# Optimization experiments

Measured on AMD Instinct MI355X. Metric: run time of the kernel, lower is better.

The kernel has to match this reference:

```python
import jax, jax.numpy as jnp
import numpy as np

TEMPERATURE = 0.1
WEIGHT = 0.1
EPS = 1e-12  # F.normalize clamp_min eps

B = 512   # number of reactions (batches)
G = 128   # atoms per reaction per side (uniform groups)
D = 256   # feature dim


def setup_inputs() -> dict:
    key = jax.random.key(0)
    k1, k2, k3, k4 = jax.random.split(key, 4)
    preds = jax.random.normal(k1, (B,), dtype=jnp.float32)
    y = jax.random.normal(k2, (B,), dtype=jnp.float32)
    reactant_features = jax.random.normal(k3, (B * G, D), dtype=jnp.float32)
    product_features = jax.random.normal(k4, (B * G, D), dtype=jnp.float32)
    # sorted, uniform-size groups: [0]*G, [1]*G, ...
    batch_idx = jnp.repeat(jnp.arange(B, dtype=jnp.int64), G)
    return {
        "preds": preds,
        "y": y,
        "reactant_features": reactant_features,
        "product_features": product_features,
        "reactant_batch_indices": batch_idx,
        "product_batch_indices": batch_idx,
    }


def _l2_normalize(x):
    # matches F.normalize(p=2, dim=1): x / max(||x||, eps)
    n = jnp.sqrt(jnp.sum(x * x, axis=-1, keepdims=True))
    return x / jnp.maximum(n, EPS)


def reference(preds, y, reactant_features, product_features,
              reactant_batch_indices, product_batch_indices):
    # MSE with reduction='sum'
    mse_loss = jnp.sum((preds - y) ** 2)

    # groups are uniform and sorted -> per-batch gather == reshape
    nb = int(reactant_batch_indices[-1]) + 1          # number of unique batches
    g = reactant_features.shape[0] // nb
    d = reactant_features.shape[1]
    r = reactant_features.reshape(nb, g, d)
    p = product_features.reshape(nb, g, d)

    rn = _l2_normalize(r)
    pn = _l2_normalize(p)
    # per-batch similarity [nb, g, g]
    sim = jnp.einsum('bgd,bhd->bgh', rn, pn) / TEMPERATURE

    # cross_entropy with labels = arange(g), mean over rows (torch default)
    lse = jax.scipy.special.logsumexp(sim, axis=-1)   # [nb, g]
    diag = jnp.einsum('bgg->bg', sim)                 # logits at true labels
    ce_per_batch = jnp.mean(lse - diag, axis=-1)      # [nb]
    contrastive_loss = jnp.mean(ce_per_batch)         # sum over batches / nb

    return mse_loss + WEIGHT * contrastive_loss
```

## Files before the change

### kernel.cpp

```cpp
#include <hip/hip_runtime.h>
#include <math.h>

#define BATCH 512
#define G 128
#define D 256
#define QROWS 32
#define LRP 264

typedef __attribute__((ext_vector_type(8))) short short8;
typedef __attribute__((ext_vector_type(4))) float f32x4;
typedef __attribute__((ext_vector_type(4))) int  i32x4;

__device__ __forceinline__ unsigned int pack2bf16(float a, float b) {
    unsigned int ua = __float_as_uint(a);
    unsigned int ub = __float_as_uint(b);
    ua = (ua + 0x7FFFu + ((ua >> 16) & 1u)) >> 16;
    ub = (ub + 0x7FFFu + ((ub >> 16) & 1u)) >> 16;
    return ua | (ub << 16);
}

__global__ __launch_bounds__(512, 4)
void fused_kernel(const float* __restrict__ rfeat,
                  const float* __restrict__ pfeat,
                  const float* __restrict__ preds,
                  const float* __restrict__ yv,
                  float* __restrict__ out)
{
    const int b = blockIdx.x;
    const float* rb = rfeat + (size_t)b * (G * D);
    const float* pb = pfeat + (size_t)b * (G * D);

    __shared__ unsigned short qs[2][QROWS * LRP];
    __shared__ float inv_r[G];
    __shared__ float inv_p[G];
    __shared__ float red[8];

    const int tid  = threadIdx.x;
    const int lane = tid & 63;
    const int wv   = tid >> 6;
    const int lg   = lane >> 4;
    const int lc   = lane & 15;

    const int srow = tid >> 4;
    const int sc4  = tid & 15;

    float4 pq0[4], pq1[4];
#pragma unroll
    for (int j = 0; j < 4; ++j)
        pq0[j] = *reinterpret_cast<const float4*>(pb + (0 * QROWS + srow) * D + (sc4 + 16 * j) * 4);
#pragma unroll
    for (int j = 0; j < 4; ++j)
        pq1[j] = *reinterpret_cast<const float4*>(pb + (1 * QROWS + srow) * D + (sc4 + 16 * j) * 4);

    short8 afr[8];
    float nrsum = 0.f;
    const float* rptr = rb + (wv * 16 + lc) * D + lg * 8;
#pragma unroll
    for (int ks = 0; ks < 8; ++ks) {
        float4 x0 = *reinterpret_cast<const float4*>(rptr + ks * 32);
        float4 x1 = *reinterpret_cast<const float4*>(rptr + ks * 32 + 4);
        nrsum += x0.x*x0.x + x0.y*x0.y + x0.z*x0.z + x0.w*x0.w
               + x1.x*x1.x + x1.y*x1.y + x1.z*x1.z + x1.w*x1.w;
        i32x4 pk = { (int)pack2bf16(x0.x, x0.y), (int)pack2bf16(x0.z, x0.w),
                     (int)pack2bf16(x1.x, x1.y), (int)pack2bf16(x1.z, x1.w) };
        union { i32x4 i; short8 s; } u; u.i = pk;
        afr[ks] = u.s;
    }
    nrsum += __shfl_xor(nrsum, 16);
    nrsum += __shfl_xor(nrsum, 32);
    if (lane < 16)
        inv_r[wv * 16 + lane] = 10.0f / fmaxf(sqrtf(nrsum), 1e-12f);

    float contrib = 0.f;
    if (b == 0) {
        float dd = preds[tid] - yv[tid];
        contrib = dd * dd;
    }

#define PACKQ(qq, buf, regs)                                                     \
    {                                                                            \
        float s_ = 0.f;                                                          \
        _Pragma("unroll")                                                        \
        for (int j = 0; j < 4; ++j) {                                            \
            const float4 v = regs[j];                                            \
            s_ += v.x*v.x + v.y*v.y + v.z*v.z + v.w*v.w;                         \
            *reinterpret_cast<uint2*>(&qs[buf][srow * LRP + (sc4 + 16 * j) * 4]) \
                = make_uint2(pack2bf16(v.x, v.y), pack2bf16(v.z, v.w));          \
        }                                                                        \
        _Pragma("unroll")                                                        \
        for (int off = 1; off < 16; off <<= 1) s_ += __shfl_xor(s_, off);        \
        if (sc4 == 0) inv_p[(qq) * QROWS + srow] = 1.0f / fmaxf(sqrtf(s_), 1e-12f); \
    }

#define CONSUME(qq, buf)                                                          \
    {                                                                             \
        _Pragma("unroll")                                                         \
        for (int ks = 0; ks < 8; ++ks) {                                          \
            const int kb = ks * 32 + lg * 8;                                      \
            short8 b0 = *reinterpret_cast<const short8*>(&qs[buf][(lc) * LRP + kb]);       \
            short8 b1 = *reinterpret_cast<const short8*>(&qs[buf][(16 + lc) * LRP + kb]);  \
            acc[2*(qq)]   = __builtin_amdgcn_mfma_f32_16x16x32_bf16(afr[ks], b0, acc[2*(qq)],   0, 0, 0); \
            acc[2*(qq)+1] = __builtin_amdgcn_mfma_f32_16x16x32_bf16(afr[ks], b1, acc[2*(qq)+1], 0, 0, 0); \
        }                                                                         \
    }

    f32x4 acc[8];
#pragma unroll
    for (int nj = 0; nj < 8; ++nj) acc[nj] = (f32x4){0.f, 0.f, 0.f, 0.f};

    PACKQ(0, 0, pq0);
    __syncthreads();

#pragma unroll
    for (int j = 0; j < 4; ++j)
        pq0[j] = *reinterpret_cast<const float4*>(pb + (2 * QROWS + srow) * D + (sc4 + 16 * j) * 4);
    CONSUME(0, 0);
    PACKQ(1, 1, pq1);
    __syncthreads();

#pragma unroll
    for (int j = 0; j < 4; ++j)
        pq1[j] = *reinterpret_cast<const float4*>(pb + (3 * QROWS + srow) * D + (sc4 + 16 * j) * 4);
    CONSUME(1, 1);
    PACKQ(2, 0, pq0);
    __syncthreads();

    CONSUME(2, 0);
    PACKQ(3, 1, pq1);
    __syncthreads();

    CONSUME(3, 1);

    float invp_r[8];
#pragma unroll
    for (int nj = 0; nj < 8; ++nj) invp_r[nj] = inv_p[nj * 16 + lc];

    const int njd = wv;
    float ce_part = 0.f;
#pragma unroll
    for (int reg = 0; reg < 4; ++reg) {
        const int rrow = lg * 4 + reg;
        const float invr_g = inv_r[wv * 16 + rrow];
        float s[8];
        float m = -3.0e38f;
#pragma unroll
        for (int nj = 0; nj < 8; ++nj) {
            s[nj] = acc[nj][reg] * invr_g * invp_r[nj];
            m = fmaxf(m, s[nj]);
        }
#pragma unroll
        for (int off = 1; off < 16; off <<= 1) m = fmaxf(m, __shfl_xor(m, off));
        float e = 0.f;
#pragma unroll
        for (int nj = 0; nj < 8; ++nj) e += __expf(s[nj] - m);
#pragma unroll
        for (int off = 1; off < 16; off <<= 1) e += __shfl_xor(e, off);
        if (lc == rrow)
            ce_part += (m + __logf(e)) - s[njd];
    }

    contrib += ce_part * (0.1f / ((float)BATCH * (float)G));
#pragma unroll
    for (int off = 1; off < 64; off <<= 1) contrib += __shfl_xor(contrib, off);
    if (lane == 0) red[wv] = contrib;
    __syncthreads();
    if (tid == 0) {
        float t = 0.f;
#pragma unroll
        for (int i = 0; i < 8; ++i) t += red[i];
        atomicAdd(out, t);
    }
#undef PACKQ
#undef CONSUME
}

extern "C" void kernel_launch(void* const* d_in, const int* in_sizes, int n_in,
                              void* d_out, int out_size, void* d_ws, size_t ws_size,
                              hipStream_t stream) {
    const float* preds = (const float*)d_in[0];
    const float* yv    = (const float*)d_in[1];
    const float* rf    = (const float*)d_in[2];
    const float* pf    = (const float*)d_in[3];
    float* out = (float*)d_out;

    hipMemsetAsync(out, 0, (size_t)out_size * sizeof(float), stream);
    fused_kernel<<<BATCH, 512, 0, stream>>>(rf, pf, preds, yv, out);
}
```

Measured before the change: 35.15 us.

## Stream product features via async global-to-LDS DMA with 4-stage ring buffer

Replaces the register-staged, bf16-packed double buffer of product rows with direct global_load_lds DMA of fp32 rows into a 4-slot, XOR-swizzled LDS ring of 16-row stages. Eight stages are consumed in turn, with the wait counts set so that three stages stay in flight. Each consumer converts fp32 to bf16 on the fly before the MFMA, and the norms are computed from LDS. The goal is to hide global load latency and free registers for more loads in flight. In exchange, LDS use grows to 64KB per block, which may limit occupancy, the bf16 conversion is now repeated across waves, and correctness depends on the manual vmcnt wait counts and raw barriers.

```diff
diff --git a/kernel.cpp b/kernel.cpp
--- a/kernel.cpp
+++ b/kernel.cpp
@@ -4,8 +4,6 @@
 #define BATCH 512
 #define G 128
 #define D 256
-#define QROWS 32
-#define LRP 264
 
 typedef __attribute__((ext_vector_type(8))) short short8;
 typedef __attribute__((ext_vector_type(4))) float f32x4;
@@ -18,6 +16,15 @@
     ub = (ub + 0x7FFFu + ((ub >> 16) & 1u)) >> 16;
     return ua | (ub << 16);
 }
+
+__device__ __forceinline__ void dma16(const float* g, float* l) {
+    __builtin_amdgcn_global_load_lds(
+        (const __attribute__((address_space(1))) void*)g,
+        (__attribute__((address_space(3))) void*)l,
+        16, 0, 0);
+}
+
+#define WAITVM(N) asm volatile("s_waitcnt vmcnt(" #N ")" ::: "memory")
 
 __global__ __launch_bounds__(512, 4)
 void fused_kernel(const float* __restrict__ rfeat,
@@ -30,7 +37,7 @@
     const float* rb = rfeat + (size_t)b * (G * D);
     const float* pb = pfeat + (size_t)b * (G * D);
 
-    __shared__ unsigned short qs[2][QROWS * LRP];
+    __shared__ float qs[4][16 * D];
     __shared__ float inv_r[G];
     __shared__ float inv_p[G];
     __shared__ float red[8];
@@ -41,24 +48,35 @@
     const int lg   = lane >> 4;
     const int lc   = lane & 15;
 
-    const int srow = tid >> 4;
-    const int sc4  = tid & 15;
-
-    float4 pq0[4], pq1[4];
-#pragma unroll
-    for (int j = 0; j < 4; ++j)
-        pq0[j] = *reinterpret_cast<const float4*>(pb + (0 * QROWS + srow) * D + (sc4 + 16 * j) * 4);
-#pragma unroll
-    for (int j = 0; j < 4; ++j)
-        pq1[j] = *reinterpret_cast<const float4*>(pb + (1 * QROWS + srow) * D + (sc4 + 16 * j) * 4);
-
+#define ISSUE(s) {                                                              \
+        _Pragma("unroll")                                                       \
+        for (int i = 0; i < 2; ++i) {                                           \
+            const int lr = 2 * wv + i;                                          \
+            const float* src = pb + ((s) * 16 + lr) * D + (lane >> 3) * 32     \
+                               + (((lane & 7) ^ (lr & 7)) << 2);               \
+            dma16(src, &qs[(s) & 3][lr * D]);                                   \
+        } }
+
+    float contrib = 0.f;
+    if (b == 0) {
+        float dd = preds[tid] - yv[tid];
+        contrib = dd * dd;
+    }
+
+    ISSUE(0); ISSUE(1); ISSUE(2);
+
+    const float* rptr = rb + (wv * 16 + lc) * D + lg * 8;
+    float4 rx[16];
+#pragma unroll
+    for (int ks = 0; ks < 8; ++ks) {
+        rx[2 * ks]     = *reinterpret_cast<const float4*>(rptr + ks * 32);
+        rx[2 * ks + 1] = *reinterpret_cast<const float4*>(rptr + ks * 32 + 4);
+    }
     short8 afr[8];
     float nrsum = 0.f;
-    const float* rptr = rb + (wv * 16 + lc) * D + lg * 8;
 #pragma unroll
     for (int ks = 0; ks < 8; ++ks) {
-        float4 x0 = *reinterpret_cast<const float4*>(rptr + ks * 32);
-        float4 x1 = *reinterpret_cast<const float4*>(rptr + ks * 32 + 4);
+        const float4 x0 = rx[2 * ks], x1 = rx[2 * ks + 1];
         nrsum += x0.x*x0.x + x0.y*x0.y + x0.z*x0.z + x0.w*x0.w
                + x1.x*x1.x + x1.y*x1.y + x1.z*x1.z + x1.w*x1.w;
         i32x4 pk = { (int)pack2bf16(x0.x, x0.y), (int)pack2bf16(x0.z, x0.w),
@@ -71,65 +89,56 @@
     if (lane < 16)
         inv_r[wv * 16 + lane] = 10.0f / fmaxf(sqrtf(nrsum), 1e-12f);
 
-    float contrib = 0.f;
-    if (b == 0) {
-        float dd = preds[tid] - yv[tid];
-        contrib = dd * dd;
-    }
-
-#define PACKQ(qq, buf, regs)                                                     \
-    {                                                                            \
-        float s_ = 0.f;                                                          \
-        _Pragma("unroll")                                                        \
-        for (int j = 0; j < 4; ++j) {                                            \
-            const float4 v = regs[j];                                            \
-            s_ += v.x*v.x + v.y*v.y + v.z*v.z + v.w*v.w;                         \
-            *reinterpret_cast<uint2*>(&qs[buf][srow * LRP + (sc4 + 16 * j) * 4]) \
-                = make_uint2(pack2bf16(v.x, v.y), pack2bf16(v.z, v.w));          \
-        }                                                                        \
-        _Pragma("unroll")                                                        \
-        for (int off = 1; off < 16; off <<= 1) s_ += __shfl_xor(s_, off);        \
-        if (sc4 == 0) inv_p[(qq) * QROWS + srow] = 1.0f / fmaxf(sqrtf(s_), 1e-12f); \
-    }
-
-#define CONSUME(qq, buf)                                                          \
-    {                                                                             \
-        _Pragma("unroll")                                                         \
-        for (int ks = 0; ks < 8; ++ks) {                                          \
-            const int kb = ks * 32 + lg * 8;                                      \
-            short8 b0 = *reinterpret_cast<const short8*>(&qs[buf][(lc) * LRP + kb]);       \
-            short8 b1 = *reinterpret_cast<const short8*>(&qs[buf][(16 + lc) * LRP + kb]);  \
-            acc[2*(qq)]   = __builtin_amdgcn_mfma_f32_16x16x32_bf16(afr[ks], b0, acc[2*(qq)],   0, 0, 0); \
-            acc[2*(qq)+1] = __builtin_amdgcn_mfma_f32_16x16x32_bf16(afr[ks], b1, acc[2*(qq)+1], 0, 0, 0); \
-        }                                                                         \
-    }
-
     f32x4 acc[8];
 #pragma unroll
     for (int nj = 0; nj < 8; ++nj) acc[nj] = (f32x4){0.f, 0.f, 0.f, 0.f};
 
-    PACKQ(0, 0, pq0);
-    __syncthreads();
-
-#pragma unroll
-    for (int j = 0; j < 4; ++j)
-        pq0[j] = *reinterpret_cast<const float4*>(pb + (2 * QROWS + srow) * D + (sc4 + 16 * j) * 4);
-    CONSUME(0, 0);
-    PACKQ(1, 1, pq1);
-    __syncthreads();
-
-#pragma unroll
-    for (int j = 0; j < 4; ++j)
-        pq1[j] = *reinterpret_cast<const float4*>(pb + (3 * QROWS + srow) * D + (sc4 + 16 * j) * 4);
-    CONSUME(1, 1);
-    PACKQ(2, 0, pq0);
-    __syncthreads();
-
-    CONSUME(2, 0);
-    PACKQ(3, 1, pq1);
-    __syncthreads();
-
-    CONSUME(3, 1);
+#define CONSUME(s) {                                                            \
+        const float* base = &qs[(s) & 3][lc * D];                               \
+        const int r7 = lc & 7;                                                  \
+        _Pragma("unroll")                                                       \
+        for (int ks = 0; ks < 8; ++ks) {                                        \
+            float4 x0 = *reinterpret_cast<const float4*>(base + ks * 32 + (((2 * lg)     ^ r7) << 2)); \
+            float4 x1 = *reinterpret_cast<const float4*>(base + ks * 32 + (((2 * lg + 1) ^ r7) << 2)); \
+            i32x4 pk = { (int)pack2bf16(x0.x, x0.y), (int)pack2bf16(x0.z, x0.w),\
+                         (int)pack2bf16(x1.x, x1.y), (int)pack2bf16(x1.z, x1.w) }; \
+            union { i32x4 i; short8 h; } u; u.i = pk;                           \
+            acc[s] = __builtin_amdgcn_mfma_f32_16x16x32_bf16(afr[ks], u.h, acc[s], 0, 0, 0); \
+        } }
+
+#define NORMS(s) {                                                              \
+        const int nrow = tid >> 5;                                              \
+        const int sc2  = tid & 31;                                              \
+        const float* np_ = &qs[(s) & 3][nrow * D + sc2 * 4];                    \
+        float4 a0 = *reinterpret_cast<const float4*>(np_);                      \
+        float4 a1 = *reinterpret_cast<const float4*>(np_ + 128);                \
+        float ss = a0.x*a0.x + a0.y*a0.y + a0.z*a0.z + a0.w*a0.w                \
+                 + a1.x*a1.x + a1.y*a1.y + a1.z*a1.z + a1.w*a1.w;               \
+        _Pragma("unroll")                                                       \
+        for (int off = 1; off < 32; off <<= 1) ss += __shfl_xor(ss, off);       \
+        if (sc2 == 0) inv_p[(s) * 16 + nrow] = 1.0f / fmaxf(sqrtf(ss), 1e-12f); \
+    }
+
+#define PHASE(s, vm, DO_ISSUE)                                                  \
+    WAITVM(vm);                                                                 \
+    __builtin_amdgcn_s_barrier();                                               \
+    asm volatile("" ::: "memory");                                              \
+    DO_ISSUE                                                                    \
+    CONSUME(s)                                                                  \
+    NORMS(s)
+
+    PHASE(0, 4, ISSUE(3))
+    PHASE(1, 4, ISSUE(4))
+    PHASE(2, 4, ISSUE(5))
+    PHASE(3, 4, ISSUE(6))
+    PHASE(4, 4, ISSUE(7))
+    PHASE(5, 4, )
+    PHASE(6, 2, )
+    PHASE(7, 0, )
+
+    asm volatile("s_waitcnt lgkmcnt(0)" ::: "memory");
+    __builtin_amdgcn_s_barrier();
+    asm volatile("" ::: "memory");
 
     float invp_r[8];
 #pragma unroll
@@ -170,8 +179,10 @@
         for (int i = 0; i < 8; ++i) t += red[i];
         atomicAdd(out, t);
     }
-#undef PACKQ
+#undef ISSUE
 #undef CONSUME
+#undef NORMS
+#undef PHASE
 }
 
 extern "C" void kernel_launch(void* const* d_in, const int* in_sizes, int n_in,
@@ -182,6 +193,7 @@
     const float* rf    = (const float*)d_in[2];
     const float* pf    = (const float*)d_in[3];
     float* out = (float*)d_out;
+    (void)d_ws; (void)ws_size;
 
     hipMemsetAsync(out, 0, (size_t)out_size * sizeof(float), stream);
     fused_kernel<<<BATCH, 512, 0, stream>>>(rf, pf, preds, yv, out);
```

After: 46.34 us. +31.9%, slower.

## Restage product tile loads into two halves with manual vmcnt waits

Applied to the files above, without the earlier changes.

Replaces the four-stage 32-row double-buffered product staging with a full 128-row bf16 shared buffer filled in two 64-row halves. All reactant loads and the first product half are issued up front, and hand-placed s_waitcnt and raw s_barrier calls let the second half's global loads overlap the first half's MFMAs. This is meant to cut the number of barriers and raise memory-level parallelism. In exchange, shared memory grows to about 66KB per block, which may reduce occupancy, and more registers are used to hold loads in flight.

```diff
diff --git a/kernel.cpp b/kernel.cpp
--- a/kernel.cpp
+++ b/kernel.cpp
@@ -4,8 +4,7 @@
 #define BATCH 512
 #define G 128
 #define D 256
-#define QROWS 32
-#define LRP 264
+#define LRB 264
 
 typedef __attribute__((ext_vector_type(8))) short short8;
 typedef __attribute__((ext_vector_type(4))) float f32x4;
@@ -18,6 +17,10 @@
     ub = (ub + 0x7FFFu + ((ub >> 16) & 1u)) >> 16;
     return ua | (ub << 16);
 }
+
+#define WAITVM(N)  asm volatile("s_waitcnt vmcnt(" #N ")" ::: "memory")
+#define WAITLGKM0  asm volatile("s_waitcnt lgkmcnt(0)" ::: "memory")
+#define FENCE      asm volatile("" ::: "memory")
 
 __global__ __launch_bounds__(512, 4)
 void fused_kernel(const float* __restrict__ rfeat,
@@ -30,7 +33,7 @@
     const float* rb = rfeat + (size_t)b * (G * D);
     const float* pb = pfeat + (size_t)b * (G * D);
 
-    __shared__ unsigned short qs[2][QROWS * LRP];
+    __shared__ unsigned short psh[G * LRB];
     __shared__ float inv_r[G];
     __shared__ float inv_p[G];
     __shared__ float red[8];
@@ -40,25 +43,57 @@
     const int wv   = tid >> 6;
     const int lg   = lane >> 4;
     const int lc   = lane & 15;
-
-    const int srow = tid >> 4;
-    const int sc4  = tid & 15;
-
-    float4 pq0[4], pq1[4];
-#pragma unroll
-    for (int j = 0; j < 4; ++j)
-        pq0[j] = *reinterpret_cast<const float4*>(pb + (0 * QROWS + srow) * D + (sc4 + 16 * j) * 4);
-#pragma unroll
-    for (int j = 0; j < 4; ++j)
-        pq1[j] = *reinterpret_cast<const float4*>(pb + (1 * QROWS + srow) * D + (sc4 + 16 * j) * 4);
-
+    const int prow = tid >> 3;
+    const int psl  = tid & 7;
+
+    float pd = 0.f, yd = 0.f;
+    if (b == 0) { pd = preds[tid]; yd = yv[tid]; }
+    FENCE;
+
+    float4 pv[8];
+#pragma unroll
+    for (int j = 0; j < 8; ++j)
+        pv[j] = *reinterpret_cast<const float4*>(pb + prow * D + (psl + 8 * j) * 4);
+    FENCE;
+
+    const float* rptr = rb + (wv * 16 + lc) * D + lg * 8;
+    float4 rx[16];
+#pragma unroll
+    for (int ks = 0; ks < 8; ++ks) {
+        rx[2 * ks]     = *reinterpret_cast<const float4*>(rptr + ks * 32);
+        rx[2 * ks + 1] = *reinterpret_cast<const float4*>(rptr + ks * 32 + 4);
+    }
+    FENCE;
+
+    WAITVM(16);
+    float contrib = 0.f;
+    if (b == 0) { float dd = pd - yd; contrib = dd * dd; }
+    {
+        float ss = 0.f;
+#pragma unroll
+        for (int j = 0; j < 8; ++j) {
+            const float4 v = pv[j];
+            ss += v.x*v.x + v.y*v.y + v.z*v.z + v.w*v.w;
+            *reinterpret_cast<uint2*>(&psh[prow * LRB + (psl + 8 * j) * 4]) =
+                make_uint2(pack2bf16(v.x, v.y), pack2bf16(v.z, v.w));
+        }
+#pragma unroll
+        for (int off = 1; off < 8; off <<= 1) ss += __shfl_xor(ss, off);
+        if (psl == 0) inv_p[prow] = 1.0f / fmaxf(sqrtf(ss), 1e-12f);
+    }
+    FENCE;
+
+#pragma unroll
+    for (int j = 0; j < 8; ++j)
+        pv[j] = *reinterpret_cast<const float4*>(pb + (64 + prow) * D + (psl + 8 * j) * 4);
+    FENCE;
+
+    WAITVM(8);
     short8 afr[8];
     float nrsum = 0.f;
-    const float* rptr = rb + (wv * 16 + lc) * D + lg * 8;
-#pragma unroll
-    for (int ks = 0; ks < 8; ++ks) {
-        float4 x0 = *reinterpret_cast<const float4*>(rptr + ks * 32);
-        float4 x1 = *reinterpret_cast<const float4*>(rptr + ks * 32 + 4);
+#pragma unroll
+    for (int ks = 0; ks < 8; ++ks) {
+        const float4 x0 = rx[2 * ks], x1 = rx[2 * ks + 1];
         nrsum += x0.x*x0.x + x0.y*x0.y + x0.z*x0.z + x0.w*x0.w
                + x1.x*x1.x + x1.y*x1.y + x1.z*x1.z + x1.w*x1.w;
         i32x4 pk = { (int)pack2bf16(x0.x, x0.y), (int)pack2bf16(x0.z, x0.w),
@@ -71,65 +106,53 @@
     if (lane < 16)
         inv_r[wv * 16 + lane] = 10.0f / fmaxf(sqrtf(nrsum), 1e-12f);
 
-    float contrib = 0.f;
-    if (b == 0) {
-        float dd = preds[tid] - yv[tid];
-        contrib = dd * dd;
-    }
-
-#define PACKQ(qq, buf, regs)                                                     \
-    {                                                                            \
-        float s_ = 0.f;                                                          \
-        _Pragma("unroll")                                                        \
-        for (int j = 0; j < 4; ++j) {                                            \
-            const float4 v = regs[j];                                            \
-            s_ += v.x*v.x + v.y*v.y + v.z*v.z + v.w*v.w;                         \
-            *reinterpret_cast<uint2*>(&qs[buf][srow * LRP + (sc4 + 16 * j) * 4]) \
-                = make_uint2(pack2bf16(v.x, v.y), pack2bf16(v.z, v.w));          \
-        }                                                                        \
-        _Pragma("unroll")                                                        \
-        for (int off = 1; off < 16; off <<= 1) s_ += __shfl_xor(s_, off);        \
-        if (sc4 == 0) inv_p[(qq) * QROWS + srow] = 1.0f / fmaxf(sqrtf(s_), 1e-12f); \
-    }
-
-#define CONSUME(qq, buf)                                                          \
-    {                                                                             \
-        _Pragma("unroll")                                                         \
-        for (int ks = 0; ks < 8; ++ks) {                                          \
-            const int kb = ks * 32 + lg * 8;                                      \
-            short8 b0 = *reinterpret_cast<const short8*>(&qs[buf][(lc) * LRP + kb]);       \
-            short8 b1 = *reinterpret_cast<const short8*>(&qs[buf][(16 + lc) * LRP + kb]);  \
-            acc[2*(qq)]   = __builtin_amdgcn_mfma_f32_16x16x32_bf16(afr[ks], b0, acc[2*(qq)],   0, 0, 0); \
-            acc[2*(qq)+1] = __builtin_amdgcn_mfma_f32_16x16x32_bf16(afr[ks], b1, acc[2*(qq)+1], 0, 0, 0); \
-        }                                                                         \
-    }
+    WAITLGKM0;
+    __builtin_amdgcn_s_barrier();
+    FENCE;
 
     f32x4 acc[8];
 #pragma unroll
     for (int nj = 0; nj < 8; ++nj) acc[nj] = (f32x4){0.f, 0.f, 0.f, 0.f};
 
-    PACKQ(0, 0, pq0);
-    __syncthreads();
-
-#pragma unroll
-    for (int j = 0; j < 4; ++j)
-        pq0[j] = *reinterpret_cast<const float4*>(pb + (2 * QROWS + srow) * D + (sc4 + 16 * j) * 4);
-    CONSUME(0, 0);
-    PACKQ(1, 1, pq1);
-    __syncthreads();
-
-#pragma unroll
-    for (int j = 0; j < 4; ++j)
-        pq1[j] = *reinterpret_cast<const float4*>(pb + (3 * QROWS + srow) * D + (sc4 + 16 * j) * 4);
-    CONSUME(1, 1);
-    PACKQ(2, 0, pq0);
-    __syncthreads();
-
-    CONSUME(2, 0);
-    PACKQ(3, 1, pq1);
-    __syncthreads();
-
-    CONSUME(3, 1);
+#pragma unroll
+    for (int ks = 0; ks < 8; ++ks) {
+        const int kb = ks * 32 + lg * 8;
+#pragma unroll
+        for (int nj = 0; nj < 4; ++nj) {
+            short8 bf = *reinterpret_cast<const short8*>(&psh[(nj * 16 + lc) * LRB + kb]);
+            acc[nj] = __builtin_amdgcn_mfma_f32_16x16x32_bf16(afr[ks], bf, acc[nj], 0, 0, 0);
+        }
+    }
+    FENCE;
+
+    WAITVM(0);
+    {
+        float ss = 0.f;
+#pragma unroll
+        for (int j = 0; j < 8; ++j) {
+            const float4 v = pv[j];
+            ss += v.x*v.x + v.y*v.y + v.z*v.z + v.w*v.w;
+            *reinterpret_cast<uint2*>(&psh[(64 + prow) * LRB + (psl + 8 * j) * 4]) =
+                make_uint2(pack2bf16(v.x, v.y), pack2bf16(v.z, v.w));
+        }
+#pragma unroll
+        for (int off = 1; off < 8; off <<= 1) ss += __shfl_xor(ss, off);
+        if (psl == 0) inv_p[64 + prow] = 1.0f / fmaxf(sqrtf(ss), 1e-12f);
+    }
+
+    WAITLGKM0;
+    __builtin_amdgcn_s_barrier();
+    FENCE;
+
+#pragma unroll
+    for (int ks = 0; ks < 8; ++ks) {
+        const int kb = ks * 32 + lg * 8;
+#pragma unroll
+        for (int nj = 4; nj < 8; ++nj) {
+            short8 bf = *reinterpret_cast<const short8*>(&psh[(nj * 16 + lc) * LRB + kb]);
+            acc[nj] = __builtin_amdgcn_mfma_f32_16x16x32_bf16(afr[ks], bf, acc[nj], 0, 0, 0);
+        }
+    }
 
     float invp_r[8];
 #pragma unroll
@@ -170,8 +193,6 @@
         for (int i = 0; i < 8; ++i) t += red[i];
         atomicAdd(out, t);
     }
-#undef PACKQ
-#undef CONSUME
 }
 
 extern "C" void kernel_launch(void* const* d_in, const int* in_sizes, int n_in,
@@ -182,6 +203,7 @@
     const float* rf    = (const float*)d_in[2];
     const float* pf    = (const float*)d_in[3];
     float* out = (float*)d_out;
+    (void)d_ws; (void)ws_size;
 
     hipMemsetAsync(out, 0, (size_t)out_size * sizeof(float), stream);
     fused_kernel<<<BATCH, 512, 0, stream>>>(rf, pf, preds, yv, out);
```

Measured after the change: 36.48 us. 3.8% more time.
